# Kernel optimization log

Measured on AMD Instinct MI355X. Metric: run time of the kernel, lower is better.

## Reference

```python
import jax, jax.numpy as jnp
import numpy as np

DIM, HEADS, HD = 256, 8, 32
WS, GT, SR = 8, 1, 2
B_, H0, W0 = 4, 128, 128
SCALE = HD ** -0.5


def _bilinear_up_align(x, s):
    # x: (B, C, h, w) -> (B, C, h*s, w*s), bilinear, align_corners=True (matches torch)
    B, C, h, w = x.shape
    oh, ow = h * s, w * s
    def coords(n, o):
        pos = jnp.arange(o, dtype=jnp.float32) * ((n - 1) / (o - 1))
        i0 = jnp.clip(jnp.floor(pos).astype(jnp.int32), 0, n - 2)
        t = pos - i0.astype(jnp.float32)
        return i0, t
    y0, ty = coords(h, oh)
    x0, tx = coords(w, ow)
    top = x[:, :, y0, :] * (1 - ty)[:, None] + x[:, :, y0 + 1, :] * ty[:, None]
    return top[:, :, :, x0] * (1 - tx) + top[:, :, :, x0 + 1] * tx


def _layernorm(x, w, b, eps=1e-5):
    mu = x.mean(-1, keepdims=True)
    var = x.var(-1, keepdims=True)
    return (x - mu) * jax.lax.rsqrt(var + eps) * w + b


def setup_inputs() -> dict:
    key = jax.random.key(0)
    ks = jax.random.split(key, 8)
    w = lambda k, shape: jax.random.normal(k, shape, jnp.float32) * 0.02
    return {
        "x": jax.random.normal(ks[0], (B_, H0 * W0, DIM), jnp.float32),
        "gt": jax.random.normal(ks[1], (B_, H0 // WS, W0 // WS, GT, DIM), jnp.float32),
        "q_w": w(ks[2], (DIM, DIM)), "q_b": jnp.zeros((DIM,), jnp.float32),
        "kv_w": w(ks[3], (2 * DIM, DIM)), "kv_b": jnp.zeros((2 * DIM,), jnp.float32),
        "sr_w": w(ks[4], (DIM, DIM, SR, SR)), "sr_b": jnp.zeros((DIM,), jnp.float32),
        "norm_w": jnp.ones((DIM,), jnp.float32), "norm_b": jnp.zeros((DIM,), jnp.float32),
        "proj_w": w(ks[5], (DIM, DIM)), "proj_b": jnp.zeros((DIM,), jnp.float32),
        "H": H0, "W": W0,
    }


def reference(x, gt, q_w, q_b, kv_w, kv_b, sr_w, sr_b, norm_w, norm_b, proj_w, proj_b, H, W):
    Bb, Np, C = x.shape
    nH, nW = H // WS, W // WS  # H, W multiples of WS -> no padding branch
    xm = x.reshape(Bb, H, W, C)
    # window partition -> (B, WS*WS, C), B = Bb*nH*nW
    xw = xm.reshape(Bb, nH, WS, nW, WS, C).transpose(0, 1, 3, 2, 4, 5).reshape(-1, WS * WS, C)
    g = gt.reshape(-1, GT, C)  # gt grid already matches (nH, nW)
    skip = g
    xc = jnp.concatenate([g, xw], axis=1)  # (B, N, C), N = GT + WS*WS
    B, N, _ = xc.shape
    q = (xc @ q_w.T + q_b).reshape(B, N, HEADS, HD).transpose(0, 2, 1, 3)  # (B,h,N,d)
    # spatial-reduction KV branch (sr_ratio > 1, gt_num != 0)
    x_ = xw.transpose(0, 2, 1).reshape(B, C, WS, WS)
    x_ = _bilinear_up_align(x_, SR)  # (B, C, WS*SR, WS*SR)
    x_ = jax.lax.conv_general_dilated(
        x_, sr_w, (SR, SR), "VALID",
        dimension_numbers=("NCHW", "OIHW", "NCHW")) + sr_b[None, :, None, None]  # (B,C,WS,WS)
    x_ = _layernorm(x_.reshape(B, C, -1).transpose(0, 2, 1), norm_w, norm_b)
    x_ = jnp.concatenate([g, x_], axis=1)  # (B, N, C)
    kv = (x_ @ kv_w.T + kv_b).reshape(B, -1, 2, HEADS, HD).transpose(2, 0, 3, 1, 4)
    k, v = kv[0], kv[1]  # (B,h,N,d)
    attn = jax.nn.softmax(jnp.einsum("bhnd,bhmd->bhnm", q, k) * SCALE, axis=-1)
    out = jnp.einsum("bhnm,bhmd->bhnd", attn, v).transpose(0, 2, 1, 3).reshape(B, N, C)
    out = out @ proj_w.T + proj_b
    gt_out = out[:, :GT, :]
    xo = out[:, GT:, :].reshape(Bb, nH, nW, WS, WS, C)
    xo = xo.transpose(0, 1, 3, 2, 4, 5).reshape(Bb, H, W, C)  # window reverse
    return xo.reshape(Bb, H * W, C), gt_out, skip
```

## Files before the change

### kernel.cpp

```cpp
#include <hip/hip_runtime.h>

typedef __attribute__((ext_vector_type(4))) float f32x4;
typedef __attribute__((ext_vector_type(8))) float f32x8;
typedef __attribute__((ext_vector_type(8))) short bf16x8;
typedef __attribute__((ext_vector_type(2))) uint u32x2;

#define SCALE_ 0.17677669529663687f

__device__ __forceinline__ float bf2f(ushort u){
  union { unsigned i; float f; } v; v.i = ((unsigned)u) << 16; return v.f;
}
__device__ __forceinline__ ushort f2bf(float f){
  union { float f; unsigned i; } v; v.f = f;
  unsigned r = v.i + 0x7fffu + ((v.i >> 16) & 1u);
  return (ushort)(r >> 16);
}
__device__ __forceinline__ void gl16(const void* g, const ushort* l) {
  __builtin_amdgcn_global_load_lds((const __attribute__((address_space(1))) uint*)g,
                                   (__attribute__((address_space(3))) uint*)l, 16, 0, 0);
}

__global__ __launch_bounds__(256) void k_prep(const float* __restrict__ x,
    const float* __restrict__ gt, ushort* __restrict__ xc,
    ushort* __restrict__ xkv, float* __restrict__ out2)
{
  int row = blockIdx.x;
  int c = threadIdx.x;
  int wi = row / 65, n = row - wi * 65;
  if (n == 0) {
    float g = gt[(size_t)wi * 256 + c];
    ushort gb = f2bf(g);
    xc[(size_t)row * 256 + c] = gb;
    xkv[(size_t)row * 256 + c] = gb;
    out2[(size_t)wi * 256 + c] = g;
  } else {
    int s = n - 1, r = s >> 3, cc = s & 7;
    int b = wi >> 8, wh = (wi >> 4) & 15, ww = wi & 15;
    int hw = (wh * 8 + r) * 128 + ww * 8 + cc;
    xc[(size_t)row * 256 + c] = f2bf(x[((size_t)b * 16384 + hw) * 256 + c]);
  }
}

__global__ __launch_bounds__(256) void k_wprep(const float* __restrict__ qw,
    const float* __restrict__ kvw, const float* __restrict__ pw,
    const float* __restrict__ srw, ushort* __restrict__ wq,
    ushort* __restrict__ wkv, ushort* __restrict__ wpr, ushort* __restrict__ wcv)
{
  int i = blockIdx.x * 256 + threadIdx.x;
  if (i < 65536)            wq[i] = f2bf(qw[i]);
  else if (i < 196608)      wkv[i - 65536] = f2bf(kvw[i - 65536]);
  else if (i < 262144)      wpr[i - 196608] = f2bf(pw[i - 196608]);
  else {
    int j = i - 262144;
    int o = j >> 10, t = (j >> 8) & 3, cc = j & 255;
    wcv[j] = f2bf(srw[o * 1024 + cc * 4 + t]);
  }
}

template<int N>
__global__ __launch_bounds__(256) void k_gemm2(const ushort* __restrict__ A,
    const ushort* __restrict__ W, const float* __restrict__ bias,
    ushort* __restrict__ C)
{
  constexpr int K = 256;
  __shared__ __align__(16) ushort As[2][128 * 64];
  __shared__ __align__(16) ushort Bs[2][128 * 64];
  int lin = blockIdx.y * gridDim.x + blockIdx.x;
  int qq = (gridDim.x * gridDim.y) >> 3;
  int sw2 = (lin & 7) * qq + (lin >> 3);
  int m0 = (sw2 / gridDim.x) * 128, n0 = (sw2 % gridDim.x) * 128;
  int tid = threadIdx.x, lane = tid & 63;
  int wave = tid >> 6;
  int lm = lane & 15, kg = lane >> 4;
  int wr = wave >> 1, wc = wave & 1;

  const char* Ab = (const char*)A + (size_t)m0 * (K * 2);
  const char* Bb = (const char*)W + (size_t)n0 * (K * 2);

  auto stage = [&](int buf, int kt) {
#pragma unroll
    for (int j = 0; j < 4; ++j) {
      int c = j * 256 + tid;
      int row = c >> 3, slot = c & 7;
      int srcoff = row * (K * 2) + kt * 128 + ((slot * 16) ^ ((row & 7) << 4));
      gl16(Ab + srcoff, (const ushort*)((const char*)As[buf] + c * 16));
      gl16(Bb + srcoff, (const ushort*)((const char*)Bs[buf] + c * 16));
    }
  };

  f32x4 acc[4][4];
  f32x4 zero = {0.f, 0.f, 0.f, 0.f};
#pragma unroll
  for (int a = 0; a < 4; ++a)
#pragma unroll
    for (int b = 0; b < 4; ++b) acc[a][b] = zero;

  stage(0, 0);
  __syncthreads();
#pragma unroll
  for (int t = 0; t < 4; ++t) {
    int cur = t & 1;
    if (t < 3) stage(cur ^ 1, t + 1);
#pragma unroll
    for (int s = 0; s < 2; ++s) {
      int sw = (lm & 7) << 4;
      bf16x8 af[4], bw[4];
#pragma unroll
      for (int mi = 0; mi < 4; ++mi) {
        int row = wr * 64 + mi * 16 + lm;
        af[mi] = *(const bf16x8*)((const char*)As[cur] + row * 128 + ((s * 64 + kg * 16) ^ sw));
      }
#pragma unroll
      for (int ni = 0; ni < 4; ++ni) {
        int row = wc * 64 + ni * 16 + lm;
        bw[ni] = *(const bf16x8*)((const char*)Bs[cur] + row * 128 + ((s * 64 + kg * 16) ^ sw));
      }
#pragma unroll
      for (int mi = 0; mi < 4; ++mi)
#pragma unroll
        for (int ni = 0; ni < 4; ++ni)
          acc[mi][ni] = __builtin_amdgcn_mfma_f32_16x16x32_bf16(af[mi], bw[ni], acc[mi][ni], 0, 0, 0);
    }
    __syncthreads();
  }

  int rbase = m0 + wr * 64 + kg * 4;
#pragma unroll
  for (int ni = 0; ni < 4; ++ni) {
    int col = n0 + wc * 64 + ni * 16 + lm;
    float bv = bias[col];
#pragma unroll
    for (int mi = 0; mi < 4; ++mi) {
#pragma unroll
      for (int r = 0; r < 4; ++r)
        C[(size_t)(rbase + mi * 16 + r) * N + col] = f2bf(acc[mi][ni][r] + bv);
    }
  }
}

__global__ __launch_bounds__(256) void k_gemm_out(const ushort* __restrict__ A,
    const ushort* __restrict__ W, const float* __restrict__ bias,
    float* __restrict__ out)
{
  constexpr int K = 256;
  __shared__ __align__(16) ushort As[2][128 * 64];
  __shared__ __align__(16) ushort Bs[2][128 * 64];
  int lin = blockIdx.y * gridDim.x + blockIdx.x;
  int qq = (gridDim.x * gridDim.y) >> 3;
  int sw2 = (lin & 7) * qq + (lin >> 3);
  int m0 = (sw2 / gridDim.x) * 128, n0 = (sw2 % gridDim.x) * 128;
  int tid = threadIdx.x, lane = tid & 63;
  int wave = tid >> 6;
  int lm = lane & 15, kg = lane >> 4;
  int wr = wave >> 1, wc = wave & 1;

  const char* Ab = (const char*)A + (size_t)m0 * (K * 2);
  const char* Bb = (const char*)W + (size_t)n0 * (K * 2);

  auto stage = [&](int buf, int kt) {
#pragma unroll
    for (int j = 0; j < 4; ++j) {
      int c = j * 256 + tid;
      int row = c >> 3, slot = c & 7;
      int srcoff = row * (K * 2) + kt * 128 + ((slot * 16) ^ ((row & 7) << 4));
      gl16(Ab + srcoff, (const ushort*)((const char*)As[buf] + c * 16));
      gl16(Bb + srcoff, (const ushort*)((const char*)Bs[buf] + c * 16));
    }
  };

  f32x4 acc[4][4];
  f32x4 zero = {0.f, 0.f, 0.f, 0.f};
#pragma unroll
  for (int a = 0; a < 4; ++a)
#pragma unroll
    for (int b = 0; b < 4; ++b) acc[a][b] = zero;

  stage(0, 0);
  __syncthreads();
#pragma unroll
  for (int t = 0; t < 4; ++t) {
    int cur = t & 1;
    if (t < 3) stage(cur ^ 1, t + 1);
#pragma unroll
    for (int s = 0; s < 2; ++s) {
      int sw = (lm & 7) << 4;
      bf16x8 af[4], bw[4];
#pragma unroll
      for (int mi = 0; mi < 4; ++mi) {
        int row = wr * 64 + mi * 16 + lm;
        af[mi] = *(const bf16x8*)((const char*)As[cur] + row * 128 + ((s * 64 + kg * 16) ^ sw));
      }
#pragma unroll
      for (int ni = 0; ni < 4; ++ni) {
        int row = wc * 64 + ni * 16 + lm;
        bw[ni] = *(const bf16x8*)((const char*)Bs[cur] + row * 128 + ((s * 64 + kg * 16) ^ sw));
      }
#pragma unroll
      for (int mi = 0; mi < 4; ++mi)
#pragma unroll
        for (int ni = 0; ni < 4; ++ni)
          acc[mi][ni] = __builtin_amdgcn_mfma_f32_16x16x32_bf16(af[mi], bw[ni], acc[mi][ni], 0, 0, 0);
    }
    __syncthreads();
  }

  int rbase = m0 + wr * 64 + kg * 4;
#pragma unroll
  for (int mi = 0; mi < 4; ++mi) {
#pragma unroll
    for (int r = 0; r < 4; ++r) {
      int g = rbase + mi * 16 + r;
      int wi2 = g / 65;
      int n = g - wi2 * 65;
      size_t dstrow;
      if (n == 0) {
        dstrow = (size_t)(16777216 >> 8) + wi2;
      } else {
        int s = n - 1;
        int b = wi2 >> 8, wh = (wi2 >> 4) & 15, ww = wi2 & 15;
        int r2 = s >> 3, cc = s & 7;
        dstrow = (size_t)(b << 14) + (wh * 8 + r2) * 128 + ww * 8 + cc;
      }
      float* dst = out + dstrow * 256;
#pragma unroll
      for (int ni = 0; ni < 4; ++ni) {
        int col = n0 + wc * 64 + ni * 16 + lm;
        dst[col] = acc[mi][ni][r] + bias[col];
      }
    }
  }
}

__device__ __forceinline__ f32x8 row_lerp(const char* srcS, int row, int cg, float ty) {
  int a0 = row * 512 + ((cg * 16) ^ ((row & 7) << 4));
  int a1 = (row + 8) * 512 + ((cg * 16) ^ ((row & 7) << 4));
  bf16x8 a = *(const bf16x8*)(srcS + a0);
  bf16x8 b = *(const bf16x8*)(srcS + a1);
  f32x8 h;
#pragma unroll
  for (int e = 0; e < 8; ++e) {
    float av = bf2f((ushort)a[e]);
    h[e] = av + ty * (bf2f((ushort)b[e]) - av);
  }
  return h;
}
__device__ __forceinline__ void emit_u(char* U, const f32x8& Ha, const f32x8& Hb,
                                       float tx, int s, int cg) {
  bf16x8 o8;
#pragma unroll
  for (int e = 0; e < 8; ++e) {
    float lv = Ha[e];
    o8[e] = (short)f2bf(lv + tx * (Hb[e] - lv));
  }
  *(bf16x8*)(U + s * 512 + ((cg * 16) ^ ((s & 7) << 4))) = o8;
}

template<int XH, int DX>
__device__ __forceinline__ void conv_build(const char* srcS, char* U,
                                           int dy, int i, int cg)
{
  int yy = 2 * i + dy;
  float py = yy * (7.0f / 15.0f);
  int iy = (int)py; if (iy > 6) iy = 6;
  float ty = py - iy;
  constexpr int j0 = XH * 3;
  int rb = iy * 8 + j0;
  f32x8 H0 = row_lerp(srcS, rb + 0, cg, ty);
  f32x8 H1 = row_lerp(srcS, rb + 1, cg, ty);
  f32x8 H2 = row_lerp(srcS, rb + 2, cg, ty);
  f32x8 H3 = row_lerp(srcS, rb + 3, cg, ty);
  f32x8 H4 = row_lerp(srcS, rb + 4, cg, ty);
  int sb = i * 8 + XH * 4;
  if (XH == 0 && DX == 0) {
    emit_u(U, H0, H1, 0.0f,        sb + 0, cg);
    emit_u(U, H0, H1, 14.f / 15.f, sb + 1, cg);
    emit_u(U, H1, H2, 13.f / 15.f, sb + 2, cg);
    emit_u(U, H2, H3, 12.f / 15.f, sb + 3, cg);
  } else if (XH == 0 && DX == 1) {
    emit_u(U, H0, H1,  7.f / 15.f, sb + 0, cg);
    emit_u(U, H1, H2,  6.f / 15.f, sb + 1, cg);
    emit_u(U, H2, H3,  5.f / 15.f, sb + 2, cg);
    emit_u(U, H3, H4,  4.f / 15.f, sb + 3, cg);
  } else if (XH == 1 && DX == 0) {
    emit_u(U, H0, H1, 11.f / 15.f, sb + 0, cg);
    emit_u(U, H1, H2, 10.f / 15.f, sb + 1, cg);
    emit_u(U, H2, H3,  9.f / 15.f, sb + 2, cg);
    emit_u(U, H3, H4,  8.f / 15.f, sb + 3, cg);
  } else {
    emit_u(U, H1, H2,  3.f / 15.f, sb + 0, cg);
    emit_u(U, H2, H3,  2.f / 15.f, sb + 1, cg);
    emit_u(U, H3, H4,  1.f / 15.f, sb + 2, cg);
    emit_u(U, H3, H4,  1.0f,       sb + 3, cg);
  }
}

__global__ __launch_bounds__(512)
__attribute__((amdgpu_waves_per_eu(4, 4)))
void k_conv(const ushort* __restrict__ xc,
    const ushort* __restrict__ wconv, ushort* __restrict__ cconv)
{
  __shared__ __align__(16) ushort srcS[64 * 256];
  __shared__ __align__(16) ushort Ubuf[64 * 256];
  int wi = blockIdx.x;
  int tid = threadIdx.x, wave = tid >> 6, lane = tid & 63;
  int lm = lane & 15, kg = lane >> 4;

  const char* src_g = (const char*)(xc + (size_t)(wi * 65 + 1) * 256);
#pragma unroll
  for (int j = 0; j < 4; ++j) {
    int c = j * 512 + tid;
    int row = c >> 5, slot = c & 31;
    int srcoff = row * 512 + ((slot * 16) ^ ((row & 7) << 4));
    gl16(src_g + srcoff, (const ushort*)((const char*)srcS + c * 16));
  }

  f32x4 acc[4][2];
  f32x4 zero = {0.f, 0.f, 0.f, 0.f};
#pragma unroll
  for (int a = 0; a < 4; a++)
#pragma unroll
    for (int b = 0; b < 2; b++) acc[a][b] = zero;

  int cg = tid & 31;
  int i = (tid >> 5) & 7;
  int xh = tid >> 8;

  auto mfma_tap = [&](int t) {
    const ushort* wc = wconv + t * 256;
    for (int kk = 0; kk < 256; kk += 32) {
      int kb = kk + kg * 8;
      bf16x8 afr[4];
#pragma unroll
      for (int mi = 0; mi < 4; mi++) {
        int srow = mi * 16 + lm;
        int off = (srow * 512 + 2 * kb) ^ ((srow & 7) << 4);
        afr[mi] = *(const bf16x8*)((const char*)Ubuf + off);
      }
#pragma unroll
      for (int ni = 0; ni < 2; ni++) {
        bf16x8 b = *(const bf16x8*)(wc + (size_t)(wave * 32 + ni * 16 + lm) * 1024 + kb);
#pragma unroll
        for (int mi = 0; mi < 4; mi++)
          acc[mi][ni] = __builtin_amdgcn_mfma_f32_16x16x32_bf16(afr[mi], b, acc[mi][ni], 0, 0, 0);
      }
    }
  };

  __syncthreads();

  if (xh == 0) conv_build<0, 0>((const char*)srcS, (char*)Ubuf, 0, i, cg);
  else         conv_build<1, 0>((const char*)srcS, (char*)Ubuf, 0, i, cg);
  __syncthreads();
  mfma_tap(0);
  __syncthreads();
  if (xh == 0) conv_build<0, 1>((const char*)srcS, (char*)Ubuf, 0, i, cg);
  else         conv_build<1, 1>((const char*)srcS, (char*)Ubuf, 0, i, cg);
  __syncthreads();
  mfma_tap(1);
  __syncthreads();
  if (xh == 0) conv_build<0, 0>((const char*)srcS, (char*)Ubuf, 1, i, cg);
  else         conv_build<1, 0>((const char*)srcS, (char*)Ubuf, 1, i, cg);
  __syncthreads();
  mfma_tap(2);
  __syncthreads();
  if (xh == 0) conv_build<0, 1>((const char*)srcS, (char*)Ubuf, 1, i, cg);
  else         conv_build<1, 1>((const char*)srcS, (char*)Ubuf, 1, i, cg);
  __syncthreads();
  mfma_tap(3);

#pragma unroll
  for (int mi = 0; mi < 4; mi++) {
    int row = wi * 64 + mi * 16 + kg * 4;
#pragma unroll
    for (int ni = 0; ni < 2; ni++) {
      int col = wave * 32 + ni * 16 + lm;
#pragma unroll
      for (int r = 0; r < 4; r++)
        cconv[(size_t)(row + r) * 256 + col] = f2bf(acc[mi][ni][r]);
    }
  }
}

__global__ __launch_bounds__(256) void k_ln(const ushort* __restrict__ cconv,
    const float* __restrict__ srb, const float* __restrict__ nw,
    const float* __restrict__ nb, ushort* __restrict__ xkv)
{
  int row = blockIdx.x * 4 + (threadIdx.x >> 6);
  int lane = threadIdx.x & 63;
  const ushort* p = cconv + (size_t)row * 256;
  float v[4]; float sum = 0.f, sq = 0.f;
#pragma unroll
  for (int r = 0; r < 4; r++) {
    int c = r * 64 + lane;
    v[r] = bf2f(p[c]) + srb[c];
    sum += v[r]; sq += v[r] * v[r];
  }
#pragma unroll
  for (int off = 1; off < 64; off <<= 1) {
    sum += __shfl_xor(sum, off, 64);
    sq  += __shfl_xor(sq,  off, 64);
  }
  float mean = sum * (1.f / 256.f);
  float var = sq * (1.f / 256.f) - mean * mean;
  float rs = rsqrtf(var + 1e-5f);
  int wi = row >> 6, s = row & 63;
  ushort* o = xkv + (size_t)(wi * 65 + 1 + s) * 256;
#pragma unroll
  for (int r = 0; r < 4; r++) {
    int c = r * 64 + lane;
    o[c] = f2bf((v[r] - mean) * rs * nw[c] + nb[c]);
  }
}

__global__ __launch_bounds__(256) void k_attn(const ushort* __restrict__ q,
    const ushort* __restrict__ kv, ushort* __restrict__ att)
{
  __shared__ ushort smem[4][8064];
  int wi = blockIdx.x >> 1;
  int tid = threadIdx.x, wave = tid >> 6, lane = tid & 63;
  int h = (blockIdx.x & 1) * 4 + wave;
  int lm = lane & 15, kg = lane >> 4;
  ushort* plds = smem[wave];
  ushort* vt   = smem[wave] + 5760;

  size_t qbase  = (size_t)wi * 65 * 256 + (size_t)h * 32;
  size_t kvbase = (size_t)wi * 65 * 512 + (size_t)h * 32;

  for (int e = lane; e < 2080; e += 64) {
    int m = e >> 5, d = e & 31;
    vt[d * 72 + m] = kv[kvbase + (size_t)m * 512 + 256 + d];
  }

  bf16x8 akf[5], bqf[5];
#pragma unroll
  for (int i = 0; i < 5; i++) {
    akf[i] = *(const bf16x8*)(kv + kvbase + (size_t)(16 * i + lm) * 512 + kg * 8);
    bqf[i] = *(const bf16x8*)(q  + qbase  + (size_t)(16 * i + lm) * 256 + kg * 8);
  }

  f32x4 sc[5][5];
  f32x4 zero = {0.f, 0.f, 0.f, 0.f};
#pragma unroll
  for (int mi = 0; mi < 5; mi++)
#pragma unroll
    for (int nj = 0; nj < 5; nj++) sc[mi][nj] = zero;
#pragma unroll
  for (int mi = 0; mi < 5; mi++)
#pragma unroll
    for (int nj = 0; nj < 5; nj++)
      sc[mi][nj] = __builtin_amdgcn_mfma_f32_16x16x32_bf16(akf[mi], bqf[nj], sc[mi][nj], 0, 0, 0);

  const float C = SCALE_ * 1.4426950408889634f;
  float inv[5], p64b[5];
#pragma unroll
  for (int nj = 0; nj < 5; nj++) {
    float s4 = sc[4][nj][0];
    float mx = (kg == 0) ? s4 : -1e30f;
#pragma unroll
    for (int mi = 0; mi < 4; mi++)
#pragma unroll
      for (int r = 0; r < 4; r++) mx = fmaxf(mx, sc[mi][nj][r]);
    mx = fmaxf(mx, __shfl_xor(mx, 16, 64));
    mx = fmaxf(mx, __shfl_xor(mx, 32, 64));
    float sum = 0.f;
#pragma unroll
    for (int mi = 0; mi < 4; mi++)
#pragma unroll
      for (int r = 0; r < 4; r++) {
        float e = exp2f((sc[mi][nj][r] - mx) * C);
        sc[mi][nj][r] = e; sum += e;
      }
    float e4 = exp2f((s4 - mx) * C);
    sum += (kg == 0) ? e4 : 0.f;
    sum += __shfl_xor(sum, 16, 64);
    sum += __shfl_xor(sum, 32, 64);
    inv[nj] = 1.0f / sum;
    p64b[nj] = __shfl(e4, lm, 64);
  }

#pragma unroll
  for (int nj = 0; nj < 5; nj++) {
    int n = 16 * nj + lm;
#pragma unroll
    for (int mi = 0; mi < 4; mi++) {
      uint lo = (uint)f2bf(sc[mi][nj][0]) | ((uint)f2bf(sc[mi][nj][1]) << 16);
      uint hi = (uint)f2bf(sc[mi][nj][2]) | ((uint)f2bf(sc[mi][nj][3]) << 16);
      u32x2 pk = {lo, hi};
      *(u32x2*)(plds + n * 72 + 16 * mi + 4 * kg) = pk;
    }
  }

  f32x4 od[2][5];
#pragma unroll
  for (int dt = 0; dt < 2; dt++)
#pragma unroll
    for (int nj = 0; nj < 5; nj++) od[dt][nj] = zero;
#pragma unroll
  for (int c = 0; c < 2; c++) {
    bf16x8 av[2], bp[5];
#pragma unroll
    for (int dt = 0; dt < 2; dt++)
      av[dt] = *(const bf16x8*)(vt + (16 * dt + lm) * 72 + c * 32 + kg * 8);
#pragma unroll
    for (int nj = 0; nj < 5; nj++)
      bp[nj] = *(const bf16x8*)(plds + (16 * nj + lm) * 72 + c * 32 + kg * 8);
#pragma unroll
    for (int dt = 0; dt < 2; dt++)
#pragma unroll
      for (int nj = 0; nj < 5; nj++)
        od[dt][nj] = __builtin_amdgcn_mfma_f32_16x16x32_bf16(av[dt], bp[nj], od[dt][nj], 0, 0, 0);
  }
  float v64[8];
#pragma unroll
  for (int dt = 0; dt < 2; dt++)
#pragma unroll
    for (int r = 0; r < 4; r++)
      v64[dt * 4 + r] = bf2f(vt[(16 * dt + 4 * kg + r) * 72 + 64]);
#pragma unroll
  for (int dt = 0; dt < 2; dt++)
#pragma unroll
    for (int nj = 0; nj < 5; nj++)
#pragma unroll
      for (int r = 0; r < 4; r++)
        od[dt][nj][r] += v64[dt * 4 + r] * p64b[nj];

#pragma unroll
  for (int nj = 0; nj < 5; nj++) {
    int n = 16 * nj + lm;
    float scl = inv[nj];
#pragma unroll
    for (int dt = 0; dt < 2; dt++) {
      uint lo = (uint)f2bf(od[dt][nj][0] * scl) | ((uint)f2bf(od[dt][nj][1] * scl) << 16);
      uint hi = (uint)f2bf(od[dt][nj][2] * scl) | ((uint)f2bf(od[dt][nj][3] * scl) << 16);
      u32x2 pk = {lo, hi};
      *(u32x2*)(plds + n * 40 + 16 * dt + 4 * kg) = pk;
    }
  }
  size_t abase = (size_t)wi * 65 * 256 + (size_t)h * 32;
  for (int e = lane; e < 1040; e += 64) {
    int n = e >> 4, d2 = e & 15;
    *(uint*)(att + abase + (size_t)n * 256 + 2 * d2) = *(const uint*)(plds + n * 40 + 2 * d2);
  }
}

extern "C" void kernel_launch(void* const* d_in, const int* in_sizes, int n_in,
                              void* d_out, int out_size, void* d_ws, size_t ws_size,
                              hipStream_t stream)
{
  const float* x    = (const float*)d_in[0];
  const float* gt   = (const float*)d_in[1];
  const float* q_w  = (const float*)d_in[2];
  const float* q_b  = (const float*)d_in[3];
  const float* kv_w = (const float*)d_in[4];
  const float* kv_b = (const float*)d_in[5];
  const float* sr_w = (const float*)d_in[6];
  const float* sr_b = (const float*)d_in[7];
  const float* nw   = (const float*)d_in[8];
  const float* nb   = (const float*)d_in[9];
  const float* p_w  = (const float*)d_in[10];
  const float* p_b  = (const float*)d_in[11];
  (void)in_sizes; (void)n_in; (void)out_size;

  if (ws_size < 204996608u) return;
  char* ws = (char*)d_ws;
  ushort* xc  = (ushort*)(ws);
  ushort* qb  = (ushort*)(ws + 34078720);
  ushort* xkv = (ushort*)(ws + 68157440);
  ushort* kv  = (ushort*)(ws + 102236160);
  ushort* ccv = (ushort*)(ws + 170393600);
  ushort* wq  = (ushort*)(ws + 203948032);
  ushort* wkv = (ushort*)(ws + 204079104);
  ushort* wpr = (ushort*)(ws + 204341248);
  ushort* wcv = (ushort*)(ws + 204472320);

  float* out = (float*)d_out;
  float* out2 = out + 16777216 + 262144;

  k_prep<<<66560, 256, 0, stream>>>(x, gt, xc, xkv, out2);
  k_wprep<<<2048, 256, 0, stream>>>(q_w, kv_w, p_w, sr_w, wq, wkv, wpr, wcv);
  k_gemm2<256><<<dim3(2, 520), 256, 0, stream>>>(xc, wq, q_b, qb);
  k_conv<<<1024, 512, 0, stream>>>(xc, wcv, ccv);
  k_ln<<<16384, 256, 0, stream>>>(ccv, sr_b, nw, nb, xkv);
  k_gemm2<512><<<dim3(4, 520), 256, 0, stream>>>(xkv, wkv, kv_b, kv);
  k_attn<<<2048, 256, 0, stream>>>(qb, kv, xc);
  k_gemm_out<<<dim3(2, 520), 256, 0, stream>>>(xc, wpr, p_b, out);
}
```

Before: 254.9 us.

## Merge weight prep into input prep and co-schedule conv with Q GEMM

Folds the weight bf16 conversion into the input prep kernel as extra blocks, which removes one launch. It also fuses the spatial-reduction conv and the Q projection GEMM into a single 512-thread kernel whose blocks alternate between conv windows and Q GEMM tiles. The aim is to cut launch overhead and let the two independent workloads overlap on the GPU. In exchange, the Q GEMM now runs with 512-thread blocks, 64KB of shared memory and a different tile schedule without the old swizzle, which may lower its efficiency.

```diff
diff --git a/kernel.cpp b/kernel.cpp
--- a/kernel.cpp
+++ b/kernel.cpp
@@ -21,10 +21,27 @@
 }
 
 __global__ __launch_bounds__(256) void k_prep(const float* __restrict__ x,
-    const float* __restrict__ gt, ushort* __restrict__ xc,
-    ushort* __restrict__ xkv, float* __restrict__ out2)
-{
-  int row = blockIdx.x;
+    const float* __restrict__ gt, const float* __restrict__ qw,
+    const float* __restrict__ kvw, const float* __restrict__ pw,
+    const float* __restrict__ srw, ushort* __restrict__ xc,
+    ushort* __restrict__ xkv, float* __restrict__ out2,
+    ushort* __restrict__ wq, ushort* __restrict__ wkv,
+    ushort* __restrict__ wpr, ushort* __restrict__ wcv)
+{
+  int blk = blockIdx.x;
+  if (blk >= 66560) {
+    int i = (blk - 66560) * 256 + threadIdx.x;
+    if (i < 65536)            wq[i] = f2bf(qw[i]);
+    else if (i < 196608)      wkv[i - 65536] = f2bf(kvw[i - 65536]);
+    else if (i < 262144)      wpr[i - 196608] = f2bf(pw[i - 196608]);
+    else {
+      int j = i - 262144;
+      int o = j >> 10, t = (j >> 8) & 3, cc = j & 255;
+      wcv[j] = f2bf(srw[o * 1024 + cc * 4 + t]);
+    }
+    return;
+  }
+  int row = blk;
   int c = threadIdx.x;
   int wi = row / 65, n = row - wi * 65;
   if (n == 0) {
@@ -38,22 +55,6 @@
     int b = wi >> 8, wh = (wi >> 4) & 15, ww = wi & 15;
     int hw = (wh * 8 + r) * 128 + ww * 8 + cc;
     xc[(size_t)row * 256 + c] = f2bf(x[((size_t)b * 16384 + hw) * 256 + c]);
-  }
-}
-
-__global__ __launch_bounds__(256) void k_wprep(const float* __restrict__ qw,
-    const float* __restrict__ kvw, const float* __restrict__ pw,
-    const float* __restrict__ srw, ushort* __restrict__ wq,
-    ushort* __restrict__ wkv, ushort* __restrict__ wpr, ushort* __restrict__ wcv)
-{
-  int i = blockIdx.x * 256 + threadIdx.x;
-  if (i < 65536)            wq[i] = f2bf(qw[i]);
-  else if (i < 196608)      wkv[i - 65536] = f2bf(kvw[i - 65536]);
-  else if (i < 262144)      wpr[i - 196608] = f2bf(pw[i - 196608]);
-  else {
-    int j = i - 262144;
-    int o = j >> 10, t = (j >> 8) & 3, cc = j & 255;
-    wcv[j] = f2bf(srw[o * 1024 + cc * 4 + t]);
   }
 }
 
@@ -294,14 +295,11 @@
   }
 }
 
-__global__ __launch_bounds__(512)
-__attribute__((amdgpu_waves_per_eu(4, 4)))
-void k_conv(const ushort* __restrict__ xc,
-    const ushort* __restrict__ wconv, ushort* __restrict__ cconv)
-{
-  __shared__ __align__(16) ushort srcS[64 * 256];
-  __shared__ __align__(16) ushort Ubuf[64 * 256];
-  int wi = blockIdx.x;
+__device__ void conv_body(int wi, const ushort* __restrict__ xc,
+    const ushort* __restrict__ wconv, ushort* __restrict__ cconv, char* smem)
+{
+  ushort* srcS = (ushort*)smem;
+  ushort* Ubuf = (ushort*)(smem + 32768);
   int tid = threadIdx.x, wave = tid >> 6, lane = tid & 63;
   int lm = lane & 15, kg = lane >> 4;
 
@@ -378,6 +376,99 @@
       for (int r = 0; r < 4; r++)
         cconv[(size_t)(row + r) * 256 + col] = f2bf(acc[mi][ni][r]);
     }
+  }
+}
+
+__device__ void gemmq_body(int idx, const ushort* __restrict__ A,
+    const ushort* __restrict__ W, const float* __restrict__ bias,
+    ushort* __restrict__ C, char* smem)
+{
+  constexpr int K = 256, N = 256;
+  ushort* As = (ushort*)smem;
+  ushort* Bs = (ushort*)(smem + 32768);
+  int gx = idx & 1, gy = idx >> 1;
+  int m0 = gy * 128, n0 = gx * 128;
+  int tid = threadIdx.x, lane = tid & 63, wave = tid >> 6;
+  int lm = lane & 15, kg = lane >> 4;
+  int wr = wave >> 2, wc = wave & 3;
+
+  const char* Ab = (const char*)A + (size_t)m0 * (K * 2);
+  const char* Bb = (const char*)W + (size_t)n0 * (K * 2);
+
+  auto stage = [&](int buf, int kt) {
+#pragma unroll
+    for (int j = 0; j < 2; ++j) {
+      int c = j * 512 + tid;
+      int row = c >> 3, slot = c & 7;
+      int srcoff = row * (K * 2) + kt * 128 + ((slot * 16) ^ ((row & 7) << 4));
+      gl16(Ab + srcoff, (const ushort*)((const char*)As + buf * 16384 + c * 16));
+      gl16(Bb + srcoff, (const ushort*)((const char*)Bs + buf * 16384 + c * 16));
+    }
+  };
+
+  f32x4 acc[4][2];
+  f32x4 zero = {0.f, 0.f, 0.f, 0.f};
+#pragma unroll
+  for (int a = 0; a < 4; ++a)
+#pragma unroll
+    for (int b = 0; b < 2; ++b) acc[a][b] = zero;
+
+  stage(0, 0);
+  __syncthreads();
+#pragma unroll
+  for (int t = 0; t < 4; ++t) {
+    int cur = t & 1;
+    if (t < 3) stage(cur ^ 1, t + 1);
+#pragma unroll
+    for (int s = 0; s < 2; ++s) {
+      int sw = (lm & 7) << 4;
+      bf16x8 af[4], bw[2];
+#pragma unroll
+      for (int mi = 0; mi < 4; ++mi) {
+        int row = wr * 64 + mi * 16 + lm;
+        af[mi] = *(const bf16x8*)((const char*)As + cur * 16384 + row * 128 + ((s * 64 + kg * 16) ^ sw));
+      }
+#pragma unroll
+      for (int ni = 0; ni < 2; ++ni) {
+        int row = wc * 32 + ni * 16 + lm;
+        bw[ni] = *(const bf16x8*)((const char*)Bs + cur * 16384 + row * 128 + ((s * 64 + kg * 16) ^ sw));
+      }
+#pragma unroll
+      for (int mi = 0; mi < 4; ++mi)
+#pragma unroll
+        for (int ni = 0; ni < 2; ++ni)
+          acc[mi][ni] = __builtin_amdgcn_mfma_f32_16x16x32_bf16(af[mi], bw[ni], acc[mi][ni], 0, 0, 0);
+    }
+    __syncthreads();
+  }
+
+  int rbase = m0 + wr * 64 + kg * 4;
+#pragma unroll
+  for (int ni = 0; ni < 2; ++ni) {
+    int col = n0 + wc * 32 + ni * 16 + lm;
+    float bv = bias[col];
+#pragma unroll
+    for (int mi = 0; mi < 4; ++mi) {
+#pragma unroll
+      for (int r = 0; r < 4; ++r)
+        C[(size_t)(rbase + mi * 16 + r) * N + col] = f2bf(acc[mi][ni][r] + bv);
+    }
+  }
+}
+
+__global__ __launch_bounds__(512)
+__attribute__((amdgpu_waves_per_eu(4, 4)))
+void k_cvq(const ushort* __restrict__ xc, const ushort* __restrict__ wconv,
+    ushort* __restrict__ cconv, const ushort* __restrict__ wq,
+    const float* __restrict__ qbias, ushort* __restrict__ qout)
+{
+  __shared__ __align__(16) char smem[65536];
+  int b = blockIdx.x;
+  if (b < 2048) {
+    if ((b & 1) == 0) conv_body(b >> 1, xc, wconv, cconv, smem);
+    else              gemmq_body(b >> 1, xc, wq, qbias, qout, smem);
+  } else {
+    gemmq_body(1024 + (b - 2048), xc, wq, qbias, qout, smem);
   }
 }
 
@@ -576,10 +667,9 @@
   float* out = (float*)d_out;
   float* out2 = out + 16777216 + 262144;
 
-  k_prep<<<66560, 256, 0, stream>>>(x, gt, xc, xkv, out2);
-  k_wprep<<<2048, 256, 0, stream>>>(q_w, kv_w, p_w, sr_w, wq, wkv, wpr, wcv);
-  k_gemm2<256><<<dim3(2, 520), 256, 0, stream>>>(xc, wq, q_b, qb);
-  k_conv<<<1024, 512, 0, stream>>>(xc, wcv, ccv);
+  k_prep<<<68608, 256, 0, stream>>>(x, gt, q_w, kv_w, p_w, sr_w,
+                                    xc, xkv, out2, wq, wkv, wpr, wcv);
+  k_cvq<<<2064, 512, 0, stream>>>(xc, wcv, ccv, wq, q_b, qb);
   k_ln<<<16384, 256, 0, stream>>>(ccv, sr_b, nw, nb, xkv);
   k_gemm2<512><<<dim3(4, 520), 256, 0, stream>>>(xkv, wkv, kv_b, kv);
   k_attn<<<2048, 256, 0, stream>>>(qb, kv, xc);
```

New measurement: 311.4 us. 22.2% more time.
